# Performance work log

Measured on AMD Instinct MI355X. Metric: run time of the kernel, lower is better.

## Reference

```python
import jax, jax.numpy as jnp
import numpy as np

EPS = 1e-8
MASK_VAL = -1.0
NEG_BIG = -1e30  # finite stand-in for -inf (fully-masked rows are overwritten later)
TEMPERATURE = 0.1


def setup_inputs() -> dict:
    key = jax.random.key(0)
    k1, k2, k3, k4 = jax.random.split(key, 4)
    B, R, W, D = 64, 36, 50, 1024
    imgs = jax.random.normal(k1, (B, R, D), dtype=jnp.float32)
    caps = jax.random.normal(k2, (B, W, D), dtype=jnp.float32)
    img_lens = jax.random.randint(k3, (B,), 1, R + 1).at[0].set(R)
    cap_lens = jax.random.randint(k4, (B,), 1, W + 1).at[0].set(W)
    alpha = jnp.array(0.5, dtype=jnp.float32)  # nn.Parameter init_alpha
    return {"imgs": imgs, "caps": caps, "img_lens": img_lens,
            "cap_lens": cap_lens, "alpha": alpha}


def _l2norm(x):
    return x / (jnp.linalg.norm(x, axis=-1, keepdims=True) + EPS)


def reference(imgs, caps, img_lens, cap_lens, alpha):
    Bi, R, D = imgs.shape
    Bc, W, _ = caps.shape
    # fine-grained cosine similarities: [Bi, Bc, R, W]
    sims = jnp.einsum('ird,cwd->icrw', _l2norm(imgs), _l2norm(caps))
    img_valid = jnp.arange(R)[None, :] < img_lens[:, None]   # [Bi, R]
    cap_valid = jnp.arange(W)[None, :] < cap_lens[:, None]   # [Bc, W]
    mask = img_valid[:, None, :, None] & cap_valid[None, :, None, :]  # [Bi,Bc,R,W]

    # hard attention: one-hot argmax over words (masked positions set to -1)
    hard_sims = jnp.where(mask, sims, MASK_VAL)
    hard_attn = jax.nn.one_hot(jnp.argmax(hard_sims, axis=-1), W, dtype=sims.dtype)
    hard_attn = jnp.where(mask, hard_attn, 0.0)

    # soft attention: masked softmax over words
    soft_attn = jax.nn.softmax(jnp.where(mask, sims / TEMPERATURE, NEG_BIG), axis=-1)
    soft_attn = jnp.where(mask, soft_attn, 0.0)

    a = jax.nn.sigmoid(alpha)
    mixed_attn = a * soft_attn + (1.0 - a) * hard_attn  # [Bi,Bc,R,W]

    # weighted caption context per (image, caption, region): [Bi,Bc,R,D]
    weighted_caps = jnp.einsum('icrw,cwd->icrd', mixed_attn, caps)
    num = jnp.einsum('icrd,ird->icr', weighted_caps, imgs)
    sims_out = num / (jnp.linalg.norm(weighted_caps, axis=-1) + EPS)  # [Bi,Bc,R]

    # final mask over invalid image regions
    return jnp.where(img_valid[:, None, :], sims_out, MASK_VAL)
```

## Files before the change

kernel.cpp:

```cpp
#include <hip/hip_runtime.h>
#include <math.h>

#define BB 64
#define RR 36
#define WW 50
#define DD 1024
#define EPSF 1e-8f

#define GM 2304
#define GN 3200
#define GK 1024

typedef __attribute__((ext_vector_type(8))) short bf16x8;
typedef __attribute__((ext_vector_type(4))) float f32x4;

#define GLL(src, dst) __builtin_amdgcn_global_load_lds( \
    (const __attribute__((address_space(1))) void*)(src), \
    (__attribute__((address_space(3))) void*)(dst), 16, 0, 0)

__device__ __forceinline__ unsigned short f2bf(float x) {
    unsigned int u = __float_as_uint(x);
    unsigned int r = (u + 0x7fffu + ((u >> 16) & 1u)) >> 16;
    return (unsigned short)r;
}
__device__ __forceinline__ float bf2f(unsigned short h) {
    return __uint_as_float(((unsigned int)h) << 16);
}

__device__ __forceinline__ int wave_sum64(const int* __restrict__ a, int lane) {
    int v = a[lane];
    #pragma unroll
    for (int off = 32; off > 0; off >>= 1) v += __shfl_xor(v, off, 64);
    return v;
}
__device__ __forceinline__ int wave_excl_at(const int* __restrict__ a, int idx, int lane) {
    int v = a[lane], inc = v;
    #pragma unroll
    for (int off = 1; off < 64; off <<= 1) {
        int t = __shfl_up(inc, off, 64);
        if (lane >= off) inc += t;
    }
    return __shfl(inc - v, idx, 64);
}

__global__ __launch_bounds__(256) void phase1_kernel(
        const float* __restrict__ imgs, const float* __restrict__ caps,
        const int* __restrict__ img_lens, const int* __restrict__ cap_lens,
        unsigned short* __restrict__ Ah, unsigned short* __restrict__ Al,
        unsigned short* __restrict__ Bh, unsigned short* __restrict__ Bl,
        float* __restrict__ invI, float* __restrict__ invC) {
    int tid = threadIdx.x;
    int lane = tid & 63, wv = tid >> 6;
    int row = blockIdx.x * 4 + wv;
    const float* X;
    unsigned short *H, *L;
    float* invN;
    size_t srcr;
    int dst;
    if (row < GM) {
        int i = row / RR, r = row - i * RR;
        if (r >= img_lens[i]) return;
        dst = wave_excl_at(img_lens, i, lane) + r;
        X = imgs; H = Ah; L = Al; invN = invI; srcr = (size_t)row;
    } else {
        int rc = row - GM;
        int c = rc / WW, w = rc - c * WW;
        if (w >= cap_lens[c]) return;
        dst = wave_excl_at(cap_lens, c, lane) + w;
        X = caps; H = Bh; L = Bl; invN = invC; srcr = (size_t)rc;
    }
    const float4* src = (const float4*)(X + srcr * DD);
    ushort4* Hd = (ushort4*)H + (size_t)dst * 256;
    ushort4* Ld = (ushort4*)L + (size_t)dst * 256;
    float ss = 0.f;
    #pragma unroll
    for (int j = 0; j < 4; j++) {
        float4 v = src[j * 64 + lane];
        float f[4] = {v.x, v.y, v.z, v.w};
        ushort4 hh, ll;
        unsigned short* hp = (unsigned short*)&hh;
        unsigned short* lp = (unsigned short*)&ll;
        #pragma unroll
        for (int jj = 0; jj < 4; jj++) {
            unsigned short hb = f2bf(f[jj]);
            hp[jj] = hb;
            lp[jj] = f2bf(f[jj] - bf2f(hb));
            ss = fmaf(f[jj], f[jj], ss);
        }
        Hd[j * 64 + lane] = hh;
        Ld[j * 64 + lane] = ll;
    }
    #pragma unroll
    for (int off = 32; off > 0; off >>= 1) ss += __shfl_down(ss, off, 64);
    if (lane == 0) invN[srcr] = 1.0f / (sqrtf(ss) + EPSF);
}

__global__ __launch_bounds__(256) void phase2_kernel(
        const unsigned short* __restrict__ Ah, const unsigned short* __restrict__ Al,
        const unsigned short* __restrict__ Bh, const unsigned short* __restrict__ Bl,
        const int* __restrict__ img_lens, const int* __restrict__ cap_lens,
        unsigned short* __restrict__ Gh, float* __restrict__ T) {
    int bid = blockIdx.x, tid = threadIdx.x;
    int lane = tid & 63, wv = tid >> 6;
    int fm = lane & 15;
    __shared__ __align__(16) unsigned short lds[4][2][4096];

    int Nsz = wave_sum64(cap_lens, lane);

    if (bid < BB) {
        int c = bid;
        int pc = wave_excl_at(cap_lens, c, lane);
        unsigned short* H16 = &lds[0][0][0];
        unsigned short* L16 = &lds[1][0][0];
        f32x4 acc[4] = {};
        for (int k0 = 0; k0 < GK; k0 += 128) {
            __syncthreads();
            #pragma unroll
            for (int j = 0; j < 4; j++) {
                int R = (wv * 4 + j) * 4 + (lane >> 4);
                int rowR = pc + R;
                if (rowR > Nsz - 1) rowR = Nsz - 1;
                int gg = (lane & 15) ^ (R & 7);
                size_t srcoff = (size_t)rowR * GK + k0 + gg * 8;
                GLL(Bh + srcoff, &H16[(wv * 4 + j) * 512]);
                GLL(Bl + srcoff, &L16[(wv * 4 + j) * 512]);
            }
            __syncthreads();
            #pragma unroll
            for (int ks = 0; ks < 4; ks++) {
                int Ra = wv * 16 + fm;
                int qa = ks * 4 + (lane >> 4);
                int oa = Ra * 128 + (qa ^ (Ra & 7)) * 8;
                bf16x8 ah = *(const bf16x8*)&H16[oa];
                bf16x8 al = *(const bf16x8*)&L16[oa];
                #pragma unroll
                for (int t = 0; t < 4; t++) {
                    int Rb = t * 16 + fm;
                    int ob = Rb * 128 + (qa ^ (Rb & 7)) * 8;
                    bf16x8 bh = *(const bf16x8*)&H16[ob];
                    bf16x8 bl = *(const bf16x8*)&L16[ob];
                    acc[t] = __builtin_amdgcn_mfma_f32_16x16x32_bf16(ah, bh, acc[t], 0, 0, 0);
                    acc[t] = __builtin_amdgcn_mfma_f32_16x16x32_bf16(ah, bl, acc[t], 0, 0, 0);
                    acc[t] = __builtin_amdgcn_mfma_f32_16x16x32_bf16(al, bh, acc[t], 0, 0, 0);
                }
            }
        }
        int row0 = wv * 16 + (lane >> 4) * 4;
        #pragma unroll
        for (int t = 0; t < 4; t++)
            #pragma unroll
            for (int v = 0; v < 4; v++)
                Gh[(size_t)c * 4096 + (row0 + v) * 64 + t * 16 + fm] = f2bf(acc[t][v]);
        return;
    }

    int q = bid - BB;
    int Msz = wave_sum64(img_lens, lane);
    int Mt = (Msz + 127) >> 7, Nt = (Nsz + 127) >> 7;
    if (q >= Mt * Nt) return;
    int m0 = (q / Nt) * 128, n0 = (q % Nt) * 128;

    int rw = (wv & 1) * 64;
    int cw = (wv >> 1) * 64;
    int srow = lane >> 2;
    int scol = ((lane & 3) ^ ((srow >> 1) & 3)) * 8;
    int fkS = ((lane >> 4) ^ ((fm >> 1) & 3)) * 8;

    f32x4 acc[4][4] = {};

    auto STAGE = [&](int buf, int kc) {
        int k0 = kc * 32;
        #pragma unroll
        for (int j = 0; j < 2; j++) {
            int seg = wv * 2 + j;
            int row = seg * 16 + srow;
            int rA = m0 + row; if (rA > Msz - 1) rA = Msz - 1;
            int rB = n0 + row; if (rB > Nsz - 1) rB = Nsz - 1;
            size_t ga = (size_t)rA * GK + k0 + scol;
            size_t gb = (size_t)rB * GK + k0 + scol;
            GLL(Ah + ga, &lds[0][buf][seg * 512]);
            GLL(Al + ga, &lds[1][buf][seg * 512]);
            GLL(Bh + gb, &lds[2][buf][seg * 512]);
            GLL(Bl + gb, &lds[3][buf][seg * 512]);
        }
    };
    auto COMPUTE = [&](int buf) {
        bf16x8 fah[4], fal[4], fbh[4], fbl[4];
        #pragma unroll
        for (int t = 0; t < 4; t++) {
            int offa = (rw + t * 16 + fm) * 32 + fkS;
            int offb = (cw + t * 16 + fm) * 32 + fkS;
            fah[t] = *(const bf16x8*)&lds[0][buf][offa];
            fal[t] = *(const bf16x8*)&lds[1][buf][offa];
            fbh[t] = *(const bf16x8*)&lds[2][buf][offb];
            fbl[t] = *(const bf16x8*)&lds[3][buf][offb];
        }
        #pragma unroll
        for (int mt = 0; mt < 4; mt++)
            #pragma unroll
            for (int nt = 0; nt < 4; nt++) {
                acc[mt][nt] = __builtin_amdgcn_mfma_f32_16x16x32_bf16(
                    fah[mt], fbh[nt], acc[mt][nt], 0, 0, 0);
                acc[mt][nt] = __builtin_amdgcn_mfma_f32_16x16x32_bf16(
                    fah[mt], fbl[nt], acc[mt][nt], 0, 0, 0);
                acc[mt][nt] = __builtin_amdgcn_mfma_f32_16x16x32_bf16(
                    fal[mt], fbh[nt], acc[mt][nt], 0, 0, 0);
            }
    };

    STAGE(0, 0);
    __syncthreads();
    int cur = 0;
    #pragma unroll 2
    for (int kc = 1; kc < 32; ++kc) {
        STAGE(cur ^ 1, kc);
        COMPUTE(cur);
        __syncthreads();
        cur ^= 1;
    }
    COMPUTE(cur);

    int orow0 = m0 + rw + (lane >> 4) * 4;
    int ocol0 = n0 + cw + fm;
    #pragma unroll
    for (int mt = 0; mt < 4; mt++)
        #pragma unroll
        for (int nt = 0; nt < 4; nt++)
            #pragma unroll
            for (int v = 0; v < 4; v++)
                T[(size_t)(orow0 + mt * 16 + v) * GN + ocol0 + nt * 16] = acc[mt][nt][v];
}

#define MST 72
__global__ __launch_bounds__(256) void epi_kernel(
        const float* __restrict__ T, const unsigned short* __restrict__ Gh,
        const int* __restrict__ img_lens, const int* __restrict__ cap_lens,
        const float* __restrict__ alpha,
        const float* __restrict__ invI, const float* __restrict__ invC,
        float* __restrict__ out) {
    int c = blockIdx.x, i = blockIdx.y;
    __shared__ __align__(16) unsigned short sGh[64 * 64];
    __shared__ __align__(16) unsigned short sMh[48 * MST];
    __shared__ __align__(16) float Hsh[36][68];
    __shared__ float numSh[36];
    __shared__ float part[36][4];

    int tid = threadIdx.x;
    int lane = tid & 63, wv = tid >> 6;
    int fm = lane & 15, fk8 = (lane >> 4) * 8;
    int hf = lane >> 5, l5 = lane & 31;

    int pI = wave_excl_at(img_lens, i, lane);
    int pC = wave_excl_at(cap_lens, c, lane);
    int lc = cap_lens[c], li = img_lens[i];

    {
        const uint4* gh = (const uint4*)(Gh + (size_t)c * 4096);
        int rowg = tid >> 3, kg = tid & 7;
        int d = (rowg << 3) | (kg ^ (rowg & 7));
        ((uint4*)sGh)[d] = gh[tid];
        ((uint4*)sGh)[d + 256] = gh[tid + 256];
    }
    for (int t = tid; t < 12 * MST; t += 256) sMh[36 * MST + t] = 0;
    __syncthreads();

    bf16x8 gfh[2];
    #pragma unroll
    for (int ks = 0; ks < 2; ks++) {
        int kg8 = ks * 4 + (lane >> 4);
        int off = (wv * 16 + fm) * 64 + (kg8 ^ (fm & 7)) * 8;
        gfh[ks] = *(const bf16x8*)&sGh[off];
    }

    float a_mix = 1.0f / (1.0f + __expf(-alpha[0]));
    float oma = 1.0f - a_mix;
    float invC0 = invC[c * WW + l5];
    float invC1 = (l5 + 32 < WW) ? invC[c * WW + l5 + 32] : 0.f;
    bool v0 = l5 < lc, v1 = (l5 + 32) < lc;

    for (int r = wv * 2 + hf; r < li; r += 8) {
        float inv_ir = invI[i * RR + r];
        const float* Trow = T + (size_t)(pI + r) * GN + pC;
        float T0 = v0 ? Trow[l5] : 0.f;
        float T1 = v1 ? Trow[l5 + 32] : 0.f;
        float S0 = v0 ? (T0 * inv_ir * invC0) : -2.f;
        float S1 = v1 ? (T1 * inv_ir * invC1) : -2.f;
        float mv; int mi;
        if (S1 > S0) { mv = S1; mi = l5 + 32; } else { mv = S0; mi = l5; }
        #pragma unroll
        for (int m = 1; m < 32; m <<= 1) {
            float ov = __shfl_xor(mv, m, 32);
            int oi = __shfl_xor(mi, m, 32);
            if (ov > mv || (ov == mv && oi < mi)) { mv = ov; mi = oi; }
        }
        float e0 = v0 ? __expf((S0 - mv) * 10.f) : 0.f;
        float e1 = v1 ? __expf((S1 - mv) * 10.f) : 0.f;
        float ss = e0 + e1, nm = fmaf(e0, T0, e1 * T1);
        #pragma unroll
        for (int m = 1; m < 32; m <<= 1) {
            ss += __shfl_xor(ss, m, 32);
            nm += __shfl_xor(nm, m, 32);
        }
        float Tmi = (mi < 32) ? __shfl(T0, mi, 32) : __shfl(T1, mi - 32, 32);
        float scale = a_mix / ss;
        float m0 = e0 * scale + (l5 == mi ? oma : 0.f);
        float m1 = e1 * scale + (l5 + 32 == mi ? oma : 0.f);
        if (l5 == 0) numSh[r] = fmaf(nm, scale, oma * Tmi);
        sMh[r * MST + l5] = f2bf(m0);
        sMh[r * MST + l5 + 32] = f2bf(m1);
    }
    __syncthreads();

    int quad4 = (lane >> 4) * 4;
    #pragma unroll
    for (int mt = 0; mt < 3; mt++) {
        f32x4 acc = {0.f, 0.f, 0.f, 0.f};
        #pragma unroll
        for (int ks = 0; ks < 2; ks++) {
            int off = (mt * 16 + fm) * MST + ks * 32 + fk8;
            bf16x8 mh = *(const bf16x8*)&sMh[off];
            acc = __builtin_amdgcn_mfma_f32_16x16x32_bf16(mh, gfh[ks], acc, 0, 0, 0);
        }
        #pragma unroll
        for (int v = 0; v < 4; v++) {
            int row = mt * 16 + quad4 + v;
            if (row < RR) Hsh[row][wv * 16 + fm] = acc[v];
        }
    }
    __syncthreads();

    if (tid < 144) {
        int r = tid >> 2, j = tid & 3;
        const bf16x8* mh = (const bf16x8*)&sMh[r * MST + j * 16];
        float p = 0.f;
        #pragma unroll
        for (int g = 0; g < 2; g++) {
            bf16x8 h8 = mh[g];
            #pragma unroll
            for (int qq = 0; qq < 8; qq++) {
                float m = bf2f((unsigned short)h8[qq]);
                p = fmaf(m, Hsh[r][j * 16 + g * 8 + qq], p);
            }
        }
        part[r][j] = p;
    }
    __syncthreads();
    if (tid < RR) {
        float den2 = part[tid][0] + part[tid][1] + part[tid][2] + part[tid][3];
        float res = (tid < li) ? (numSh[tid] / (sqrtf(den2) + EPSF)) : -1.0f;
        out[((size_t)i * BB + c) * RR + tid] = res;
    }
}

extern "C" void kernel_launch(void* const* d_in, const int* in_sizes, int n_in,
                              void* d_out, int out_size, void* d_ws, size_t ws_size,
                              hipStream_t stream) {
    const float* imgs = (const float*)d_in[0];
    const float* caps = (const float*)d_in[1];
    const int* img_lens = (const int*)d_in[2];
    const int* cap_lens = (const int*)d_in[3];
    const float* alpha = (const float*)d_in[4];
    float* out = (float*)d_out;

    float* ws = (float*)d_ws;
    float* invI = ws;
    float* invC = ws + BB * RR;
    float* T = invC + BB * WW;
    unsigned short* Ah = (unsigned short*)(T + (size_t)GM * GN);
    unsigned short* Al = Ah + (size_t)GM * GK;
    unsigned short* Bh = Al + (size_t)GM * GK;
    unsigned short* Bl = Bh + (size_t)GN * GK;
    unsigned short* Gbh = Bl + (size_t)GN * GK;

    phase1_kernel<<<(GM + GN) / 4, 256, 0, stream>>>(
        imgs, caps, img_lens, cap_lens, Ah, Al, Bh, Bl, invI, invC);
    phase2_kernel<<<BB + 450, 256, 0, stream>>>(
        Ah, Al, Bh, Bl, img_lens, cap_lens, Gbh, T);
    epi_kernel<<<dim3(BB, BB), 256, 0, stream>>>(
        T, Gbh, img_lens, cap_lens, alpha, invI, invC, out);
}
```

Before: 127.2 us.

## Triple-buffer GEMM LDS staging with explicit vmcnt waits and barriers

Reorganizes the phase2 GEMM's LDS into three stage buffers and issues global-to-LDS loads two k-steps ahead of compute. Waits use s_waitcnt vmcnt(8) and a raw barrier instead of __syncthreads, so one stage of loads can stay in flight while the current stage is computed. This aims to hide global load latency better. In exchange it uses more shared memory per block, which may lower occupancy, and the hand-counted vmcnt must match the number of loads issued per stage.

```diff
diff --git a/kernel.cpp b/kernel.cpp
--- a/kernel.cpp
+++ b/kernel.cpp
@@ -103,7 +103,7 @@
     int bid = blockIdx.x, tid = threadIdx.x;
     int lane = tid & 63, wv = tid >> 6;
     int fm = lane & 15;
-    __shared__ __align__(16) unsigned short lds[4][2][4096];
+    __shared__ __align__(16) unsigned short lds[3][4][4096];
 
     int Nsz = wave_sum64(cap_lens, lane);
 
@@ -111,7 +111,7 @@
         int c = bid;
         int pc = wave_excl_at(cap_lens, c, lane);
         unsigned short* H16 = &lds[0][0][0];
-        unsigned short* L16 = &lds[1][0][0];
+        unsigned short* L16 = &lds[0][2][0];
         f32x4 acc[4] = {};
         for (int k0 = 0; k0 < GK; k0 += 128) {
             __syncthreads();
@@ -178,10 +178,10 @@
             int rB = n0 + row; if (rB > Nsz - 1) rB = Nsz - 1;
             size_t ga = (size_t)rA * GK + k0 + scol;
             size_t gb = (size_t)rB * GK + k0 + scol;
-            GLL(Ah + ga, &lds[0][buf][seg * 512]);
-            GLL(Al + ga, &lds[1][buf][seg * 512]);
-            GLL(Bh + gb, &lds[2][buf][seg * 512]);
-            GLL(Bl + gb, &lds[3][buf][seg * 512]);
+            GLL(Ah + ga, &lds[buf][0][seg * 512]);
+            GLL(Al + ga, &lds[buf][1][seg * 512]);
+            GLL(Bh + gb, &lds[buf][2][seg * 512]);
+            GLL(Bl + gb, &lds[buf][3][seg * 512]);
         }
     };
     auto COMPUTE = [&](int buf) {
@@ -190,10 +190,10 @@
         for (int t = 0; t < 4; t++) {
             int offa = (rw + t * 16 + fm) * 32 + fkS;
             int offb = (cw + t * 16 + fm) * 32 + fkS;
-            fah[t] = *(const bf16x8*)&lds[0][buf][offa];
-            fal[t] = *(const bf16x8*)&lds[1][buf][offa];
-            fbh[t] = *(const bf16x8*)&lds[2][buf][offb];
-            fbl[t] = *(const bf16x8*)&lds[3][buf][offb];
+            fah[t] = *(const bf16x8*)&lds[buf][0][offa];
+            fal[t] = *(const bf16x8*)&lds[buf][1][offa];
+            fbh[t] = *(const bf16x8*)&lds[buf][2][offb];
+            fbl[t] = *(const bf16x8*)&lds[buf][3][offb];
         }
         #pragma unroll
         for (int mt = 0; mt < 4; mt++)
@@ -208,17 +208,30 @@
             }
     };
 
+    #define KSTEP_WAIT(N) do { \
+        asm volatile("s_waitcnt vmcnt(" #N ")" ::: "memory"); \
+        __builtin_amdgcn_s_barrier(); \
+        asm volatile("" ::: "memory"); \
+    } while (0)
+
     STAGE(0, 0);
-    __syncthreads();
-    int cur = 0;
-    #pragma unroll 2
-    for (int kc = 1; kc < 32; ++kc) {
-        STAGE(cur ^ 1, kc);
-        COMPUTE(cur);
-        __syncthreads();
-        cur ^= 1;
-    }
-    COMPUTE(cur);
+    STAGE(1, 1);
+    for (int u = 0; u < 10; ++u) {
+        KSTEP_WAIT(8);
+        STAGE(2, 3 * u + 2);
+        COMPUTE(0);
+        KSTEP_WAIT(8);
+        STAGE(0, 3 * u + 3);
+        COMPUTE(1);
+        KSTEP_WAIT(8);
+        STAGE(1, 3 * u + 4);
+        COMPUTE(2);
+    }
+    KSTEP_WAIT(8);
+    COMPUTE(0);
+    KSTEP_WAIT(0);
+    COMPUTE(1);
+    #undef KSTEP_WAIT
 
     int orow0 = m0 + rw + (lane >> 4) * 4;
     int ocol0 = n0 + cw + fm;
```

Measured after the change: 125.9 us (median of 2 runs). Within noise of the previous version (-1.0%).

## Split GEMM K dimension three ways with partial-sum slices reduced in epilogue

Applied to the files above, without the earlier changes.

The main GEMM in phase2 is split along K into three chunks (11/11/10 of 32 k-steps). Each chunk writes a separate partial-sum slice of T, and the epilogue adds the three slices when it reads T. This triples the number of GEMM tiles so more of the GPU's compute units are busy when the tile count is small. In exchange it triples the T workspace and its write and read traffic, and drops the unroll pragma.

```diff
diff --git a/kernel.cpp b/kernel.cpp
--- a/kernel.cpp
+++ b/kernel.cpp
@@ -10,6 +10,7 @@
 #define GM 2304
 #define GN 3200
 #define GK 1024
+#define TSL ((size_t)GM * GN)
 
 typedef __attribute__((ext_vector_type(8))) short bf16x8;
 typedef __attribute__((ext_vector_type(4))) float f32x4;
@@ -157,8 +158,13 @@
     int q = bid - BB;
     int Msz = wave_sum64(img_lens, lane);
     int Mt = (Msz + 127) >> 7, Nt = (Nsz + 127) >> 7;
-    if (q >= Mt * Nt) return;
-    int m0 = (q / Nt) * 128, n0 = (q % Nt) * 128;
+    int ntile = Mt * Nt;
+    if (q >= 3 * ntile) return;
+    int s = q / ntile;
+    int t = q - s * ntile;
+    int m0 = (t / Nt) * 128, n0 = (t % Nt) * 128;
+    int kbeg = s * 11, kcnt = (s == 2) ? 10 : 11;
+    float* Ts = T + (size_t)s * TSL;
 
     int rw = (wv & 1) * 64;
     int cw = (wv >> 1) * 64;
@@ -187,13 +193,13 @@
     auto COMPUTE = [&](int buf) {
         bf16x8 fah[4], fal[4], fbh[4], fbl[4];
         #pragma unroll
-        for (int t = 0; t < 4; t++) {
-            int offa = (rw + t * 16 + fm) * 32 + fkS;
-            int offb = (cw + t * 16 + fm) * 32 + fkS;
-            fah[t] = *(const bf16x8*)&lds[0][buf][offa];
-            fal[t] = *(const bf16x8*)&lds[1][buf][offa];
-            fbh[t] = *(const bf16x8*)&lds[2][buf][offb];
-            fbl[t] = *(const bf16x8*)&lds[3][buf][offb];
+        for (int t2 = 0; t2 < 4; t2++) {
+            int offa = (rw + t2 * 16 + fm) * 32 + fkS;
+            int offb = (cw + t2 * 16 + fm) * 32 + fkS;
+            fah[t2] = *(const bf16x8*)&lds[0][buf][offa];
+            fal[t2] = *(const bf16x8*)&lds[1][buf][offa];
+            fbh[t2] = *(const bf16x8*)&lds[2][buf][offb];
+            fbl[t2] = *(const bf16x8*)&lds[3][buf][offb];
         }
         #pragma unroll
         for (int mt = 0; mt < 4; mt++)
@@ -208,12 +214,11 @@
             }
     };
 
-    STAGE(0, 0);
+    STAGE(0, kbeg);
     __syncthreads();
     int cur = 0;
-    #pragma unroll 2
-    for (int kc = 1; kc < 32; ++kc) {
-        STAGE(cur ^ 1, kc);
+    for (int kc = 1; kc < kcnt; ++kc) {
+        STAGE(cur ^ 1, kbeg + kc);
         COMPUTE(cur);
         __syncthreads();
         cur ^= 1;
@@ -228,7 +233,7 @@
         for (int nt = 0; nt < 4; nt++)
             #pragma unroll
             for (int v = 0; v < 4; v++)
-                T[(size_t)(orow0 + mt * 16 + v) * GN + ocol0 + nt * 16] = acc[mt][nt][v];
+                Ts[(size_t)(orow0 + mt * 16 + v) * GN + ocol0 + nt * 16] = acc[mt][nt][v];
 }
 
 #define MST 72
@@ -281,8 +286,8 @@
     for (int r = wv * 2 + hf; r < li; r += 8) {
         float inv_ir = invI[i * RR + r];
         const float* Trow = T + (size_t)(pI + r) * GN + pC;
-        float T0 = v0 ? Trow[l5] : 0.f;
-        float T1 = v1 ? Trow[l5 + 32] : 0.f;
+        float T0 = v0 ? (Trow[l5] + Trow[l5 + TSL] + Trow[l5 + 2 * TSL]) : 0.f;
+        float T1 = v1 ? (Trow[l5 + 32] + Trow[l5 + 32 + TSL] + Trow[l5 + 32 + 2 * TSL]) : 0.f;
         float S0 = v0 ? (T0 * inv_ir * invC0) : -2.f;
         float S1 = v1 ? (T1 * inv_ir * invC1) : -2.f;
         float mv; int mi;
@@ -366,7 +371,7 @@
     float* invI = ws;
     float* invC = ws + BB * RR;
     float* T = invC + BB * WW;
-    unsigned short* Ah = (unsigned short*)(T + (size_t)GM * GN);
+    unsigned short* Ah = (unsigned short*)(T + 3 * TSL);
     unsigned short* Al = Ah + (size_t)GM * GK;
     unsigned short* Bh = Al + (size_t)GM * GK;
     unsigned short* Bl = Bh + (size_t)GN * GK;
@@ -374,7 +379,7 @@
 
     phase1_kernel<<<(GM + GN) / 4, 256, 0, stream>>>(
         imgs, caps, img_lens, cap_lens, Ah, Al, Bh, Bl, invI, invC);
-    phase2_kernel<<<BB + 450, 256, 0, stream>>>(
+    phase2_kernel<<<BB + 3 * 450, 256, 0, stream>>>(
         Ah, Al, Bh, Bl, img_lens, cap_lens, Gbh, T);
     epi_kernel<<<dim3(BB, BB), 256, 0, stream>>>(
         T, Gbh, img_lens, cap_lens, alpha, invI, invC, out);
```

Result: slower. 131.0 us (+3.0%).
